# Kernel tuning notes

Hardware: AMD Instinct MI355X
Metric: run time of the kernel (lower is better)

The kernel has to match this reference:

```python
import jax, jax.numpy as jnp
import numpy as np

IN_DIM = 256
HID = 512
PAT = 10
B = 512
BN_EPS = 1e-5


def setup_inputs() -> dict:
    key = jax.random.key(0)
    ks = jax.random.split(key, 16)
    s = 0.05
    return {
        "x": jax.random.normal(ks[0], (B, IN_DIM), jnp.float32),
        # pattern_detector params
        "W1": jax.random.normal(ks[1], (HID, IN_DIM), jnp.float32) * s,
        "b1": jax.random.normal(ks[2], (HID,), jnp.float32) * s,
        "bn_gamma": 1.0 + jax.random.normal(ks[3], (HID,), jnp.float32) * s,
        "bn_beta": jax.random.normal(ks[4], (HID,), jnp.float32) * s,
        "bn_mean": jax.random.normal(ks[5], (HID,), jnp.float32) * s,
        "bn_var": jnp.ones((HID,), jnp.float32),
        "W2": jax.random.normal(ks[6], (HID // 2, HID), jnp.float32) * s,
        "b2": jax.random.normal(ks[7], (HID // 2,), jnp.float32) * s,
        "W3": jax.random.normal(ks[8], (PAT, HID // 2), jnp.float32) * s,
        "b3": jax.random.normal(ks[9], (PAT,), jnp.float32) * s,
        # similarity_layer params; first Linear weight [HID, 2*IN_DIM] split into
        # the half acting on x_i (Ws1_a) and the half acting on x_j (Ws1_b)
        "Ws1_a": jax.random.normal(ks[10], (HID, IN_DIM), jnp.float32) * s,
        "Ws1_b": jax.random.normal(ks[11], (HID, IN_DIM), jnp.float32) * s,
        "bs1": jax.random.normal(ks[12], (HID,), jnp.float32) * s,
        "ws2": jax.random.normal(ks[13], (HID,), jnp.float32) * s,
        "bs2": jax.random.normal(ks[14], (), jnp.float32) * s,
    }


def reference(x, W1, b1, bn_gamma, bn_beta, bn_mean, bn_var, W2, b2, W3, b3,
              Ws1_a, Ws1_b, bs1, ws2, bs2):
    # --- pattern_detector MLP (eval mode: BN uses running stats, dropout off) ---
    h = x @ W1.T + b1                                    # [B, HID]
    h = bn_gamma * (h - bn_mean) * jax.lax.rsqrt(bn_var + BN_EPS) + bn_beta
    h = jax.nn.relu(h)
    h2 = jax.nn.relu(h @ W2.T + b2)                      # [B, HID//2]
    pattern_scores = h2 @ W3.T + b3                      # [B, PAT]
    pattern_probs = jax.nn.softmax(pattern_scores, axis=-1)

    # --- pairwise similarity: sim(i,j) = MLP(concat(x_i, x_j)) ---
    # Linear([x_i; x_j]) = x_i @ Ws1_a^T + x_j @ Ws1_b^T + bs1, so precompute
    # the two GEMMs and broadcast-add instead of materializing [B,B,2*IN_DIM].
    A = x @ Ws1_a.T                                      # [B, HID]
    C = x @ Ws1_b.T                                      # [B, HID]
    hid = jax.nn.relu(A[:, None, :] + C[None, :, :] + bs1)  # [B, B, HID]
    logits = hid @ ws2 + bs2                             # [B, B]
    sim_full = jax.nn.sigmoid(logits)
    # Original loops i<j only and mirrors, diagonal stays 0. Results are
    # detached (.item()) in torch, so stop_gradient for faithfulness.
    iu = jnp.triu(jnp.ones((x.shape[0], x.shape[0]), sim_full.dtype), k=1)
    S = sim_full * iu
    similarities = jax.lax.stop_gradient(S + S.T)

    return pattern_probs, pattern_scores, similarities
```

## Files before the change

kernel.cpp:

```cpp
#include <hip/hip_runtime.h>
#include <math.h>

#define BN_EPS 1e-5f

typedef _Float16 half2v __attribute__((ext_vector_type(2)));
typedef _Float16 half8v __attribute__((ext_vector_type(8)));
typedef __fp16 fp16x8 __attribute__((ext_vector_type(8)));
typedef float floatx4 __attribute__((ext_vector_type(4)));

__device__ __forceinline__ float fdot2(half2v a, half2v b, float c) {
    return __builtin_amdgcn_fdot2(a, b, c, false);
}
__device__ __forceinline__ half2v cvt2(float a, float b) {
    return __builtin_bit_cast(half2v, __builtin_amdgcn_cvt_pkrtz(a, b));
}
__device__ __forceinline__ floatx4 mfma16(half8v a, half8v b, floatx4 c) {
    return __builtin_amdgcn_mfma_f32_16x16x32_f16(
        __builtin_bit_cast(fp16x8, a), __builtin_bit_cast(fp16x8, b), c, 0, 0, 0);
}
__device__ __forceinline__ half2v h2sub(half8v v, int s) {
    return __builtin_shufflevector(v, v, 0, 1);
}

__global__ __launch_bounds__(256) void fused3_mfma(
    const float* __restrict__ x,
    const float* __restrict__ W1, const float* __restrict__ b1,
    const float* __restrict__ g, const float* __restrict__ be,
    const float* __restrict__ mu, const float* __restrict__ va,
    const float* __restrict__ Wa, const float* __restrict__ bs1,
    const float* __restrict__ Wb,
    _Float16* __restrict__ h16, _Float16* __restrict__ A16,
    _Float16* __restrict__ C16)
{
    __shared__ _Float16 Xs[64][264];
    __shared__ _Float16 Ws[32][264];

    const int t  = threadIdx.x;
    const int n0 = blockIdx.x * 32;
    const int m0 = blockIdx.y * 64;
    const int z  = blockIdx.z;
    const float* __restrict__ Wp = (z == 0) ? W1 : (z == 1 ? Wa : Wb);

    #pragma unroll
    for (int i = 0; i < 16; ++i) {
        const int cidx = t + i * 256;
        const int row = cidx >> 6;
        const int c4  = cidx & 63;
        const float4 v = *(const float4*)&x[(m0 + row) * 256 + c4 * 4];
        *(half2v*)&Xs[row][c4 * 4 + 0] = cvt2(v.x, v.y);
        *(half2v*)&Xs[row][c4 * 4 + 2] = cvt2(v.z, v.w);
    }
    #pragma unroll
    for (int i = 0; i < 8; ++i) {
        const int cidx = t + i * 256;
        const int row = cidx >> 6;
        const int c4  = cidx & 63;
        const float4 v = *(const float4*)&Wp[(n0 + row) * 256 + c4 * 4];
        *(half2v*)&Ws[row][c4 * 4 + 0] = cvt2(v.x, v.y);
        *(half2v*)&Ws[row][c4 * 4 + 2] = cvt2(v.z, v.w);
    }
    __syncthreads();

    const int wave = t >> 6;
    const int lane = t & 63;
    const int wy = wave >> 1, wx = wave & 1;
    const int lrow = lane & 15;
    const int quad = lane >> 4;
    const int kq = quad * 8;

    floatx4 acc[2] = {{0.f, 0.f, 0.f, 0.f}, {0.f, 0.f, 0.f, 0.f}};

    #pragma unroll
    for (int kc = 0; kc < 256; kc += 32) {
        const half8v a0 = *(const half8v*)&Xs[wy * 32 + lrow][kc + kq];
        const half8v a1 = *(const half8v*)&Xs[wy * 32 + 16 + lrow][kc + kq];
        const half8v b0 = *(const half8v*)&Ws[wx * 16 + lrow][kc + kq];
        acc[0] = mfma16(a0, b0, acc[0]);
        acc[1] = mfma16(a1, b0, acc[1]);
    }

    const int n = n0 + wx * 16 + lrow;
    float scale, off;
    if (z == 0) {
        const float s = g[n] * rsqrtf(va[n] + BN_EPS);
        scale = s;
        off = (b1[n] - mu[n]) * s + be[n];
    } else if (z == 1) {
        scale = 1.f;
        off = bs1[n];
    } else {
        scale = 1.f;
        off = 0.f;
    }
    _Float16* __restrict__ dst = (z == 0) ? h16 : (z == 1 ? A16 : C16);
    #pragma unroll
    for (int mi = 0; mi < 2; ++mi) {
        #pragma unroll
        for (int r = 0; r < 4; ++r) {
            const int m = m0 + wy * 32 + mi * 16 + quad * 4 + r;
            float v = acc[mi][r] * scale + off;
            if (z == 0) v = fmaxf(v, 0.f);
            dst[m * 512 + n] = (_Float16)v;
        }
    }
}

__global__ __launch_bounds__(512) void h2sim_kernel(
    const _Float16* __restrict__ h16, const float* __restrict__ W2,
    const float* __restrict__ b2, float* __restrict__ h2o,
    const _Float16* __restrict__ A16, const _Float16* __restrict__ C16,
    const float* __restrict__ ws2, const float* __restrict__ bs2,
    float* __restrict__ S)
{
    __shared__ __align__(16) char smem[78080];
    const int bid = blockIdx.x;
    const int t   = threadIdx.x;

    if (bid < 128) {
        _Float16* Xs = (_Float16*)smem;
        _Float16* Ws = Xs + 32 * 520;
        float*    Ph = (float*)(smem + 66560);

        const int n0 = (bid & 7) * 32;
        const int m0 = (bid >> 3) * 32;

        #pragma unroll
        for (int i = 0; i < 4; ++i) {
            const int c = t + i * 512;
            const int row = c >> 6;
            const int c8  = c & 63;
            const float4 v = *(const float4*)&h16[(m0 + row) * 512 + c8 * 8];
            *(half8v*)&Xs[row * 520 + c8 * 8] = __builtin_bit_cast(half8v, v);
        }
        #pragma unroll
        for (int i = 0; i < 4; ++i) {
            const int c = t + i * 512;
            const int row = c >> 6;
            const int c8  = c & 63;
            const float4 v0 = *(const float4*)&W2[(n0 + row) * 512 + c8 * 8];
            const float4 v1 = *(const float4*)&W2[(n0 + row) * 512 + c8 * 8 + 4];
            _Float16* d = &Ws[row * 520 + c8 * 8];
            *(half2v*)(d + 0) = cvt2(v0.x, v0.y);
            *(half2v*)(d + 2) = cvt2(v0.z, v0.w);
            *(half2v*)(d + 4) = cvt2(v1.x, v1.y);
            *(half2v*)(d + 6) = cvt2(v1.z, v1.w);
        }
        __syncthreads();

        const int wave = t >> 6;
        const int lane = t & 63;
        const int gk = wave >> 2;
        const int wl = wave & 3;
        const int wy = wl >> 1, wx = wl & 1;
        const int lrow = lane & 15;
        const int quad = lane >> 4;
        const int kq = quad * 8;
        const int kb = gk * 256;

        floatx4 acc = {0.f, 0.f, 0.f, 0.f};
        #pragma unroll
        for (int kc = 0; kc < 256; kc += 32) {
            const half8v a = *(const half8v*)&Xs[(wy * 16 + lrow) * 520 + kb + kc + kq];
            const half8v b = *(const half8v*)&Ws[(wx * 16 + lrow) * 520 + kb + kc + kq];
            acc = mfma16(a, b, acc);
        }

        if (gk == 1) {
            #pragma unroll
            for (int r = 0; r < 4; ++r)
                Ph[(wy * 16 + quad * 4 + r) * 33 + wx * 16 + lrow] = acc[r];
        }
        __syncthreads();
        if (gk == 0) {
            const int n = n0 + wx * 16 + lrow;
            const float bb = b2[n];
            #pragma unroll
            for (int r = 0; r < 4; ++r) {
                const int ml = wy * 16 + quad * 4 + r;
                h2o[(m0 + ml) * 256 + n] =
                    fmaxf(acc[r] + Ph[ml * 33 + wx * 16 + lrow] + bb, 0.f);
            }
        }
        return;
    }

    _Float16* Rs = (_Float16*)smem;
    _Float16* Qs = Rs + 32 * 536;
    half2v*  wsh = (half2v*)(smem + 68608);
    float*   Psf = (float*)(smem + 68608 + 1024);
    float*   Tt  = Psf + 32 * 33;

    const int b = bid - 128;
    int jt = 0;
    while ((jt + 1) * (jt + 2) / 2 <= b) ++jt;
    const int it = b - jt * (jt + 1) / 2;
    const int r0 = it * 32, q0 = jt * 32;
    const bool diag = (it == jt);

    const int gk = t >> 8;
    const int tl = t & 255;
    const int tx = tl & 15, ty = tl >> 4;

    if (t < 256) {
        half2v w;
        w.x = (_Float16)ws2[2 * t];
        w.y = (_Float16)ws2[2 * t + 1];
        wsh[t] = w;
    }
    #pragma unroll
    for (int i = 0; i < 4; ++i) {
        const int c = t + i * 512;
        const int row = c >> 6;
        const int c8  = c & 63;
        const float4 vr = *(const float4*)&A16[(r0 + row) * 512 + c8 * 8];
        const float4 vq = *(const float4*)&C16[(q0 + row) * 512 + c8 * 8];
        *(half8v*)&Rs[row * 536 + c8 * 8] = __builtin_bit_cast(half8v, vr);
        *(half8v*)&Qs[row * 536 + c8 * 8] = __builtin_bit_cast(half8v, vq);
    }
    __syncthreads();

    const int cb = gk * 32;
    const half8v* rp0 = (const half8v*)&Rs[(ty * 2 + 0) * 536];
    const half8v* rp1 = (const half8v*)&Rs[(ty * 2 + 1) * 536];
    const half8v* qp0 = (const half8v*)&Qs[(tx * 2 + 0) * 536];
    const half8v* qp1 = (const half8v*)&Qs[(tx * 2 + 1) * 536];
    const half8v* wp8 = (const half8v*)wsh;
    const half2v z2 = {(_Float16)0, (_Float16)0};

    float a00 = 0.f, a01 = 0.f, a10 = 0.f, a11 = 0.f;
    #pragma unroll 4
    for (int c = 0; c < 32; ++c) {
        const half8v r0c = rp0[cb + c];
        const half8v r1c = rp1[cb + c];
        const half8v q0c = qp0[cb + c];
        const half8v q1c = qp1[cb + c];
        const half8v wc  = wp8[cb + c];
        #pragma unroll
        for (int s = 0; s < 4; ++s) {
            half2v r0s, r1s, q0s, q1s, wss;
            switch (s) {
            case 0: r0s = __builtin_shufflevector(r0c, r0c, 0, 1);
                    r1s = __builtin_shufflevector(r1c, r1c, 0, 1);
                    q0s = __builtin_shufflevector(q0c, q0c, 0, 1);
                    q1s = __builtin_shufflevector(q1c, q1c, 0, 1);
                    wss = __builtin_shufflevector(wc, wc, 0, 1); break;
            case 1: r0s = __builtin_shufflevector(r0c, r0c, 2, 3);
                    r1s = __builtin_shufflevector(r1c, r1c, 2, 3);
                    q0s = __builtin_shufflevector(q0c, q0c, 2, 3);
                    q1s = __builtin_shufflevector(q1c, q1c, 2, 3);
                    wss = __builtin_shufflevector(wc, wc, 2, 3); break;
            case 2: r0s = __builtin_shufflevector(r0c, r0c, 4, 5);
                    r1s = __builtin_shufflevector(r1c, r1c, 4, 5);
                    q0s = __builtin_shufflevector(q0c, q0c, 4, 5);
                    q1s = __builtin_shufflevector(q1c, q1c, 4, 5);
                    wss = __builtin_shufflevector(wc, wc, 4, 5); break;
            default: r0s = __builtin_shufflevector(r0c, r0c, 6, 7);
                    r1s = __builtin_shufflevector(r1c, r1c, 6, 7);
                    q0s = __builtin_shufflevector(q0c, q0c, 6, 7);
                    q1s = __builtin_shufflevector(q1c, q1c, 6, 7);
                    wss = __builtin_shufflevector(wc, wc, 6, 7); break;
            }
            a00 = fdot2(__builtin_elementwise_max(r0s + q0s, z2), wss, a00);
            a01 = fdot2(__builtin_elementwise_max(r0s + q1s, z2), wss, a01);
            a10 = fdot2(__builtin_elementwise_max(r1s + q0s, z2), wss, a10);
            a11 = fdot2(__builtin_elementwise_max(r1s + q1s, z2), wss, a11);
        }
    }

    if (gk == 1) {
        Psf[(ty * 2 + 0) * 33 + tx * 2 + 0] = a00;
        Psf[(ty * 2 + 0) * 33 + tx * 2 + 1] = a01;
        Psf[(ty * 2 + 1) * 33 + tx * 2 + 0] = a10;
        Psf[(ty * 2 + 1) * 33 + tx * 2 + 1] = a11;
    }
    __syncthreads();

    if (gk == 0) {
        const float bsv = bs2[0];
        float v[2][2];
        v[0][0] = a00 + Psf[(ty * 2 + 0) * 33 + tx * 2 + 0];
        v[0][1] = a01 + Psf[(ty * 2 + 0) * 33 + tx * 2 + 1];
        v[1][0] = a10 + Psf[(ty * 2 + 1) * 33 + tx * 2 + 0];
        v[1][1] = a11 + Psf[(ty * 2 + 1) * 33 + tx * 2 + 1];
        #pragma unroll
        for (int di = 0; di < 2; ++di)
            #pragma unroll
            for (int dj = 0; dj < 2; ++dj) {
                v[di][dj] = 1.f / (1.f + __expf(-(v[di][dj] + bsv)));
                Tt[(ty * 2 + di) * 33 + tx * 2 + dj] = v[di][dj];
            }
        if (!diag) {
            #pragma unroll
            for (int di = 0; di < 2; ++di)
                *(float2*)&S[(r0 + ty * 2 + di) * 512 + q0 + tx * 2] =
                    make_float2(v[di][0], v[di][1]);
        }
    }
    __syncthreads();

    if (gk == 0) {
        if (diag) {
            #pragma unroll
            for (int di = 0; di < 2; ++di)
                #pragma unroll
                for (int dj = 0; dj < 2; ++dj) {
                    const int rl = ty * 2 + di, ql = tx * 2 + dj;
                    const float o = rl < ql ? Tt[rl * 33 + ql]
                                  : (rl > ql ? Tt[ql * 33 + rl] : 0.f);
                    S[(r0 + rl) * 512 + q0 + ql] = o;
                }
        } else {
            #pragma unroll
            for (int di = 0; di < 2; ++di)
                #pragma unroll
                for (int dj = 0; dj < 2; ++dj)
                    S[(q0 + ty * 2 + di) * 512 + r0 + tx * 2 + dj] =
                        Tt[(tx * 2 + dj) * 33 + ty * 2 + di];
        }
    }
}

__global__ __launch_bounds__(256) void head_kernel(
    const float* __restrict__ h2, const float* __restrict__ W3,
    const float* __restrict__ b3, float* __restrict__ out)
{
    const int t = threadIdx.x;
    const int lane = t & 63;
    const int r = blockIdx.x * 4 + (t >> 6);

    float p[10];
    #pragma unroll
    for (int q = 0; q < 10; ++q) p[q] = 0.f;
    #pragma unroll
    for (int kk = 0; kk < 4; ++kk) {
        const int k = lane + kk * 64;
        const float hv = h2[r * 256 + k];
        #pragma unroll
        for (int q = 0; q < 10; ++q)
            p[q] = fmaf(hv, W3[q * 256 + k], p[q]);
    }
    #pragma unroll
    for (int q = 0; q < 10; ++q) {
        #pragma unroll
        for (int off = 32; off > 0; off >>= 1)
            p[q] += __shfl_down(p[q], off);
    }
    if (lane == 0) {
        float s[10], m = -1e30f;
        #pragma unroll
        for (int q = 0; q < 10; ++q) { s[q] = p[q] + b3[q]; m = fmaxf(m, s[q]); }
        float e[10], sum = 0.f;
        #pragma unroll
        for (int q = 0; q < 10; ++q) { e[q] = __expf(s[q] - m); sum += e[q]; }
        const float inv = 1.f / sum;
        #pragma unroll
        for (int q = 0; q < 10; ++q) {
            out[r * 10 + q] = e[q] * inv;
            out[5120 + r * 10 + q] = s[q];
        }
    }
}

extern "C" void kernel_launch(void* const* d_in, const int* in_sizes, int n_in,
                              void* d_out, int out_size, void* d_ws, size_t ws_size,
                              hipStream_t stream)
{
    const float* x   = (const float*)d_in[0];
    const float* W1  = (const float*)d_in[1];
    const float* b1  = (const float*)d_in[2];
    const float* g   = (const float*)d_in[3];
    const float* be  = (const float*)d_in[4];
    const float* mu  = (const float*)d_in[5];
    const float* va  = (const float*)d_in[6];
    const float* W2  = (const float*)d_in[7];
    const float* b2  = (const float*)d_in[8];
    const float* W3  = (const float*)d_in[9];
    const float* b3  = (const float*)d_in[10];
    const float* Wa  = (const float*)d_in[11];
    const float* Wb  = (const float*)d_in[12];
    const float* bs1 = (const float*)d_in[13];
    const float* ws2 = (const float*)d_in[14];
    const float* bs2 = (const float*)d_in[15];

    float* out = (float*)d_out;
    _Float16* h16 = (_Float16*)d_ws;
    float* h2 = (float*)(h16 + 512 * 512);
    _Float16* A16 = (_Float16*)(h2 + 512 * 256);
    _Float16* C16 = A16 + 512 * 512;

    fused3_mfma<<<dim3(16, 8, 3), 256, 0, stream>>>(x, W1, b1, g, be, mu, va,
                                                    Wa, bs1, Wb, h16, A16, C16);
    h2sim_kernel<<<264, 512, 0, stream>>>(h16, W2, b2, h2, A16, C16, ws2, bs2,
                                          out + 10240);
    head_kernel<<<128, 256, 0, stream>>>(h2, W3, b3, out);
}
```

Baseline: 101.7 us.

## Merge three kernels into one cooperative kernel with grid-wide syncs

Replaces the three separate launches (projection GEMMs, h2+similarity, head) with one cooperative mega-kernel of 256 blocks that uses grid.sync between phases. The first phase is retiled to 64x64 output tiles over 192 blocks. The second phase loops over its 264 jobs with 256 blocks, so 8 blocks run two jobs. The goal is to remove kernel launch gaps. In exchange it adds grid-barrier cost, a serialized tail in phase two, and a dependence on all 256 blocks of 512 threads with about 78KB of shared memory being co-resident.

After: 285.8 us. +181.0%, slower.

```diff
diff --git a/kernel.cpp b/kernel.cpp
--- a/kernel.cpp
+++ b/kernel.cpp
@@ -1,5 +1,8 @@
 #include <hip/hip_runtime.h>
+#include <hip/hip_cooperative_groups.h>
 #include <math.h>
+
+namespace cg = cooperative_groups;
 
 #define BN_EPS 1e-5f
 
@@ -18,345 +21,344 @@
     return __builtin_amdgcn_mfma_f32_16x16x32_f16(
         __builtin_bit_cast(fp16x8, a), __builtin_bit_cast(fp16x8, b), c, 0, 0, 0);
 }
-__device__ __forceinline__ half2v h2sub(half8v v, int s) {
-    return __builtin_shufflevector(v, v, 0, 1);
-}
-
-__global__ __launch_bounds__(256) void fused3_mfma(
+
+__global__ __launch_bounds__(512) void mega_kernel(
     const float* __restrict__ x,
     const float* __restrict__ W1, const float* __restrict__ b1,
     const float* __restrict__ g, const float* __restrict__ be,
     const float* __restrict__ mu, const float* __restrict__ va,
     const float* __restrict__ Wa, const float* __restrict__ bs1,
     const float* __restrict__ Wb,
+    const float* __restrict__ W2, const float* __restrict__ b2,
+    const float* __restrict__ W3, const float* __restrict__ b3,
+    const float* __restrict__ ws2, const float* __restrict__ bs2,
     _Float16* __restrict__ h16, _Float16* __restrict__ A16,
-    _Float16* __restrict__ C16)
-{
-    __shared__ _Float16 Xs[64][264];
-    __shared__ _Float16 Ws[32][264];
-
-    const int t  = threadIdx.x;
-    const int n0 = blockIdx.x * 32;
-    const int m0 = blockIdx.y * 64;
-    const int z  = blockIdx.z;
-    const float* __restrict__ Wp = (z == 0) ? W1 : (z == 1 ? Wa : Wb);
-
-    #pragma unroll
-    for (int i = 0; i < 16; ++i) {
-        const int cidx = t + i * 256;
-        const int row = cidx >> 6;
-        const int c4  = cidx & 63;
-        const float4 v = *(const float4*)&x[(m0 + row) * 256 + c4 * 4];
-        *(half2v*)&Xs[row][c4 * 4 + 0] = cvt2(v.x, v.y);
-        *(half2v*)&Xs[row][c4 * 4 + 2] = cvt2(v.z, v.w);
-    }
-    #pragma unroll
-    for (int i = 0; i < 8; ++i) {
-        const int cidx = t + i * 256;
-        const int row = cidx >> 6;
-        const int c4  = cidx & 63;
-        const float4 v = *(const float4*)&Wp[(n0 + row) * 256 + c4 * 4];
-        *(half2v*)&Ws[row][c4 * 4 + 0] = cvt2(v.x, v.y);
-        *(half2v*)&Ws[row][c4 * 4 + 2] = cvt2(v.z, v.w);
-    }
-    __syncthreads();
-
-    const int wave = t >> 6;
-    const int lane = t & 63;
-    const int wy = wave >> 1, wx = wave & 1;
-    const int lrow = lane & 15;
-    const int quad = lane >> 4;
-    const int kq = quad * 8;
-
-    floatx4 acc[2] = {{0.f, 0.f, 0.f, 0.f}, {0.f, 0.f, 0.f, 0.f}};
-
-    #pragma unroll
-    for (int kc = 0; kc < 256; kc += 32) {
-        const half8v a0 = *(const half8v*)&Xs[wy * 32 + lrow][kc + kq];
-        const half8v a1 = *(const half8v*)&Xs[wy * 32 + 16 + lrow][kc + kq];
-        const half8v b0 = *(const half8v*)&Ws[wx * 16 + lrow][kc + kq];
-        acc[0] = mfma16(a0, b0, acc[0]);
-        acc[1] = mfma16(a1, b0, acc[1]);
-    }
-
-    const int n = n0 + wx * 16 + lrow;
-    float scale, off;
-    if (z == 0) {
-        const float s = g[n] * rsqrtf(va[n] + BN_EPS);
-        scale = s;
-        off = (b1[n] - mu[n]) * s + be[n];
-    } else if (z == 1) {
-        scale = 1.f;
-        off = bs1[n];
-    } else {
-        scale = 1.f;
-        off = 0.f;
-    }
-    _Float16* __restrict__ dst = (z == 0) ? h16 : (z == 1 ? A16 : C16);
-    #pragma unroll
-    for (int mi = 0; mi < 2; ++mi) {
-        #pragma unroll
-        for (int r = 0; r < 4; ++r) {
-            const int m = m0 + wy * 32 + mi * 16 + quad * 4 + r;
-            float v = acc[mi][r] * scale + off;
-            if (z == 0) v = fmaxf(v, 0.f);
-            dst[m * 512 + n] = (_Float16)v;
-        }
-    }
-}
-
-__global__ __launch_bounds__(512) void h2sim_kernel(
-    const _Float16* __restrict__ h16, const float* __restrict__ W2,
-    const float* __restrict__ b2, float* __restrict__ h2o,
-    const _Float16* __restrict__ A16, const _Float16* __restrict__ C16,
-    const float* __restrict__ ws2, const float* __restrict__ bs2,
-    float* __restrict__ S)
+    _Float16* __restrict__ C16, float* __restrict__ h2o,
+    float* __restrict__ out)
 {
     __shared__ __align__(16) char smem[78080];
     const int bid = blockIdx.x;
     const int t   = threadIdx.x;
-
-    if (bid < 128) {
+    cg::grid_group grid = cg::this_grid();
+
+    if (bid < 192) {
         _Float16* Xs = (_Float16*)smem;
-        _Float16* Ws = Xs + 32 * 520;
-        float*    Ph = (float*)(smem + 66560);
-
-        const int n0 = (bid & 7) * 32;
-        const int m0 = (bid >> 3) * 32;
-
-        #pragma unroll
-        for (int i = 0; i < 4; ++i) {
+        _Float16* Ws = Xs + 64 * 264;
+        const int z   = bid / 64;
+        const int rem = bid % 64;
+        const int m0 = (rem >> 3) * 64;
+        const int n0 = (rem & 7) * 64;
+        const float* __restrict__ Wp = (z == 0) ? W1 : (z == 1 ? Wa : Wb);
+
+        #pragma unroll
+        for (int i = 0; i < 8; ++i) {
             const int c = t + i * 512;
             const int row = c >> 6;
-            const int c8  = c & 63;
-            const float4 v = *(const float4*)&h16[(m0 + row) * 512 + c8 * 8];
-            *(half8v*)&Xs[row * 520 + c8 * 8] = __builtin_bit_cast(half8v, v);
-        }
-        #pragma unroll
-        for (int i = 0; i < 4; ++i) {
+            const int c4  = c & 63;
+            const float4 v = *(const float4*)&x[(m0 + row) * 256 + c4 * 4];
+            *(half2v*)&Xs[row * 264 + c4 * 4 + 0] = cvt2(v.x, v.y);
+            *(half2v*)&Xs[row * 264 + c4 * 4 + 2] = cvt2(v.z, v.w);
+        }
+        #pragma unroll
+        for (int i = 0; i < 8; ++i) {
             const int c = t + i * 512;
             const int row = c >> 6;
-            const int c8  = c & 63;
-            const float4 v0 = *(const float4*)&W2[(n0 + row) * 512 + c8 * 8];
-            const float4 v1 = *(const float4*)&W2[(n0 + row) * 512 + c8 * 8 + 4];
-            _Float16* d = &Ws[row * 520 + c8 * 8];
-            *(half2v*)(d + 0) = cvt2(v0.x, v0.y);
-            *(half2v*)(d + 2) = cvt2(v0.z, v0.w);
-            *(half2v*)(d + 4) = cvt2(v1.x, v1.y);
-            *(half2v*)(d + 6) = cvt2(v1.z, v1.w);
+            const int c4  = c & 63;
+            const float4 v = *(const float4*)&Wp[(n0 + row) * 256 + c4 * 4];
+            *(half2v*)&Ws[row * 264 + c4 * 4 + 0] = cvt2(v.x, v.y);
+            *(half2v*)&Ws[row * 264 + c4 * 4 + 2] = cvt2(v.z, v.w);
         }
         __syncthreads();
 
         const int wave = t >> 6;
         const int lane = t & 63;
-        const int gk = wave >> 2;
-        const int wl = wave & 3;
-        const int wy = wl >> 1, wx = wl & 1;
+        const int wy = wave >> 2, wx = wave & 3;
         const int lrow = lane & 15;
         const int quad = lane >> 4;
         const int kq = quad * 8;
-        const int kb = gk * 256;
-
-        floatx4 acc = {0.f, 0.f, 0.f, 0.f};
+
+        floatx4 acc[2] = {{0.f, 0.f, 0.f, 0.f}, {0.f, 0.f, 0.f, 0.f}};
         #pragma unroll
         for (int kc = 0; kc < 256; kc += 32) {
-            const half8v a = *(const half8v*)&Xs[(wy * 16 + lrow) * 520 + kb + kc + kq];
-            const half8v b = *(const half8v*)&Ws[(wx * 16 + lrow) * 520 + kb + kc + kq];
-            acc = mfma16(a, b, acc);
-        }
-
-        if (gk == 1) {
-            #pragma unroll
-            for (int r = 0; r < 4; ++r)
-                Ph[(wy * 16 + quad * 4 + r) * 33 + wx * 16 + lrow] = acc[r];
-        }
+            const half8v a0 = *(const half8v*)&Xs[(wy * 32 + lrow) * 264 + kc + kq];
+            const half8v a1 = *(const half8v*)&Xs[(wy * 32 + 16 + lrow) * 264 + kc + kq];
+            const half8v b0 = *(const half8v*)&Ws[(wx * 16 + lrow) * 264 + kc + kq];
+            acc[0] = mfma16(a0, b0, acc[0]);
+            acc[1] = mfma16(a1, b0, acc[1]);
+        }
+
+        const int n = n0 + wx * 16 + lrow;
+        float scale, off;
+        if (z == 0) {
+            const float s = g[n] * rsqrtf(va[n] + BN_EPS);
+            scale = s;
+            off = (b1[n] - mu[n]) * s + be[n];
+        } else if (z == 1) {
+            scale = 1.f;
+            off = bs1[n];
+        } else {
+            scale = 1.f;
+            off = 0.f;
+        }
+        _Float16* __restrict__ dst = (z == 0) ? h16 : (z == 1 ? A16 : C16);
+        #pragma unroll
+        for (int mi = 0; mi < 2; ++mi) {
+            #pragma unroll
+            for (int r = 0; r < 4; ++r) {
+                const int m = m0 + wy * 32 + mi * 16 + quad * 4 + r;
+                float v = acc[mi][r] * scale + off;
+                if (z == 0) v = fmaxf(v, 0.f);
+                dst[m * 512 + n] = (_Float16)v;
+            }
+        }
+    }
+
+    __threadfence();
+    grid.sync();
+
+    float* __restrict__ S = out + 10240;
+    for (int job = bid; job < 264; job += 256) {
         __syncthreads();
-        if (gk == 0) {
-            const int n = n0 + wx * 16 + lrow;
-            const float bb = b2[n];
-            #pragma unroll
-            for (int r = 0; r < 4; ++r) {
-                const int ml = wy * 16 + quad * 4 + r;
-                h2o[(m0 + ml) * 256 + n] =
-                    fmaxf(acc[r] + Ph[ml * 33 + wx * 16 + lrow] + bb, 0.f);
-            }
-        }
-        return;
+        if (job < 128) {
+            _Float16* Xs = (_Float16*)smem;
+            _Float16* Ws = Xs + 32 * 520;
+            float*    Ph = (float*)(smem + 66560);
+
+            const int n0 = (job & 7) * 32;
+            const int m0 = (job >> 3) * 32;
+
+            #pragma unroll
+            for (int i = 0; i < 4; ++i) {
+                const int c = t + i * 512;
+                const int row = c >> 6;
+                const int c8  = c & 63;
+                const float4 v = *(const float4*)&h16[(m0 + row) * 512 + c8 * 8];
+                *(half8v*)&Xs[row * 520 + c8 * 8] = __builtin_bit_cast(half8v, v);
+            }
+            #pragma unroll
+            for (int i = 0; i < 4; ++i) {
+                const int c = t + i * 512;
+                const int row = c >> 6;
+                const int c8  = c & 63;
+                const float4 v0 = *(const float4*)&W2[(n0 + row) * 512 + c8 * 8];
+                const float4 v1 = *(const float4*)&W2[(n0 + row) * 512 + c8 * 8 + 4];
+                _Float16* d = &Ws[row * 520 + c8 * 8];
+                *(half2v*)(d + 0) = cvt2(v0.x, v0.y);
+                *(half2v*)(d + 2) = cvt2(v0.z, v0.w);
+                *(half2v*)(d + 4) = cvt2(v1.x, v1.y);
+                *(half2v*)(d + 6) = cvt2(v1.z, v1.w);
+            }
+            __syncthreads();
+
+            const int wave = t >> 6;
+            const int lane = t & 63;
+            const int gk = wave >> 2;
+            const int wl = wave & 3;
+            const int wy = wl >> 1, wx = wl & 1;
+            const int lrow = lane & 15;
+            const int quad = lane >> 4;
+            const int kq = quad * 8;
+            const int kb = gk * 256;
+
+            floatx4 acc = {0.f, 0.f, 0.f, 0.f};
+            #pragma unroll
+            for (int kc = 0; kc < 256; kc += 32) {
+                const half8v a = *(const half8v*)&Xs[(wy * 16 + lrow) * 520 + kb + kc + kq];
+                const half8v b = *(const half8v*)&Ws[(wx * 16 + lrow) * 520 + kb + kc + kq];
+                acc = mfma16(a, b, acc);
+            }
+
+            if (gk == 1) {
+                #pragma unroll
+                for (int r = 0; r < 4; ++r)
+                    Ph[(wy * 16 + quad * 4 + r) * 33 + wx * 16 + lrow] = acc[r];
+            }
+            __syncthreads();
+            if (gk == 0) {
+                const int n = n0 + wx * 16 + lrow;
+                const float bb = b2[n];
+                #pragma unroll
+                for (int r = 0; r < 4; ++r) {
+                    const int ml = wy * 16 + quad * 4 + r;
+                    h2o[(m0 + ml) * 256 + n] =
+                        fmaxf(acc[r] + Ph[ml * 33 + wx * 16 + lrow] + bb, 0.f);
+                }
+            }
+        } else {
+            _Float16* Rs = (_Float16*)smem;
+            _Float16* Qs = Rs + 32 * 536;
+            half2v*  wsh = (half2v*)(smem + 68608);
+            float*   Psf = (float*)(smem + 68608 + 1024);
+            float*   Tt  = Psf + 32 * 33;
+
+            const int b = job - 128;
+            int jt = 0;
+            while ((jt + 1) * (jt + 2) / 2 <= b) ++jt;
+            const int it = b - jt * (jt + 1) / 2;
+            const int r0 = it * 32, q0 = jt * 32;
+            const bool diag = (it == jt);
+
+            const int gk = t >> 8;
+            const int tl = t & 255;
+            const int tx = tl & 15, ty = tl >> 4;
+
+            if (t < 256) {
+                half2v w;
+                w.x = (_Float16)ws2[2 * t];
+                w.y = (_Float16)ws2[2 * t + 1];
+                wsh[t] = w;
+            }
+            #pragma unroll
+            for (int i = 0; i < 4; ++i) {
+                const int c = t + i * 512;
+                const int row = c >> 6;
+                const int c8  = c & 63;
+                const float4 vr = *(const float4*)&A16[(r0 + row) * 512 + c8 * 8];
+                const float4 vq = *(const float4*)&C16[(q0 + row) * 512 + c8 * 8];
+                *(half8v*)&Rs[row * 536 + c8 * 8] = __builtin_bit_cast(half8v, vr);
+                *(half8v*)&Qs[row * 536 + c8 * 8] = __builtin_bit_cast(half8v, vq);
+            }
+            __syncthreads();
+
+            const int cb = gk * 32;
+            const half8v* rp0 = (const half8v*)&Rs[(ty * 2 + 0) * 536];
+            const half8v* rp1 = (const half8v*)&Rs[(ty * 2 + 1) * 536];
+            const half8v* qp0 = (const half8v*)&Qs[(tx * 2 + 0) * 536];
+            const half8v* qp1 = (const half8v*)&Qs[(tx * 2 + 1) * 536];
+            const half8v* wp8 = (const half8v*)wsh;
+            const half2v z2 = {(_Float16)0, (_Float16)0};
+
+            float a00 = 0.f, a01 = 0.f, a10 = 0.f, a11 = 0.f;
+            #pragma unroll 4
+            for (int c = 0; c < 32; ++c) {
+                const half8v r0c = rp0[cb + c];
+                const half8v r1c = rp1[cb + c];
+                const half8v q0c = qp0[cb + c];
+                const half8v q1c = qp1[cb + c];
+                const half8v wc  = wp8[cb + c];
+                #pragma unroll
+                for (int s = 0; s < 4; ++s) {
+                    half2v r0s, r1s, q0s, q1s, wss;
+                    switch (s) {
+                    case 0: r0s = __builtin_shufflevector(r0c, r0c, 0, 1);
+                            r1s = __builtin_shufflevector(r1c, r1c, 0, 1);
+                            q0s = __builtin_shufflevector(q0c, q0c, 0, 1);
+                            q1s = __builtin_shufflevector(q1c, q1c, 0, 1);
+                            wss = __builtin_shufflevector(wc, wc, 0, 1); break;
+                    case 1: r0s = __builtin_shufflevector(r0c, r0c, 2, 3);
+                            r1s = __builtin_shufflevector(r1c, r1c, 2, 3);
+                            q0s = __builtin_shufflevector(q0c, q0c, 2, 3);
+                            q1s = __builtin_shufflevector(q1c, q1c, 2, 3);
+                            wss = __builtin_shufflevector(wc, wc, 2, 3); break;
+                    case 2: r0s = __builtin_shufflevector(r0c, r0c, 4, 5);
+                            r1s = __builtin_shufflevector(r1c, r1c, 4, 5);
+                            q0s = __builtin_shufflevector(q0c, q0c, 4, 5);
+                            q1s = __builtin_shufflevector(q1c, q1c, 4, 5);
+                            wss = __builtin_shufflevector(wc, wc, 4, 5); break;
+                    default: r0s = __builtin_shufflevector(r0c, r0c, 6, 7);
+                            r1s = __builtin_shufflevector(r1c, r1c, 6, 7);
+                            q0s = __builtin_shufflevector(q0c, q0c, 6, 7);
+                            q1s = __builtin_shufflevector(q1c, q1c, 6, 7);
+                            wss = __builtin_shufflevector(wc, wc, 6, 7); break;
+                    }
+                    a00 = fdot2(__builtin_elementwise_max(r0s + q0s, z2), wss, a00);
+                    a01 = fdot2(__builtin_elementwise_max(r0s + q1s, z2), wss, a01);
+                    a10 = fdot2(__builtin_elementwise_max(r1s + q0s, z2), wss, a10);
+                    a11 = fdot2(__builtin_elementwise_max(r1s + q1s, z2), wss, a11);
+                }
+            }
+
+            if (gk == 1) {
+                Psf[(ty * 2 + 0) * 33 + tx * 2 + 0] = a00;
+                Psf[(ty * 2 + 0) * 33 + tx * 2 + 1] = a01;
+                Psf[(ty * 2 + 1) * 33 + tx * 2 + 0] = a10;
+                Psf[(ty * 2 + 1) * 33 + tx * 2 + 1] = a11;
+            }
+            __syncthreads();
+
+            if (gk == 0) {
+                const float bsv = bs2[0];
+                float v[2][2];
+                v[0][0] = a00 + Psf[(ty * 2 + 0) * 33 + tx * 2 + 0];
+                v[0][1] = a01 + Psf[(ty * 2 + 0) * 33 + tx * 2 + 1];
+                v[1][0] = a10 + Psf[(ty * 2 + 1) * 33 + tx * 2 + 0];
+                v[1][1] = a11 + Psf[(ty * 2 + 1) * 33 + tx * 2 + 1];
+                #pragma unroll
+                for (int di = 0; di < 2; ++di)
+                    #pragma unroll
+                    for (int dj = 0; dj < 2; ++dj) {
+                        v[di][dj] = 1.f / (1.f + __expf(-(v[di][dj] + bsv)));
+                        Tt[(ty * 2 + di) * 33 + tx * 2 + dj] = v[di][dj];
+                    }
+                if (!diag) {
+                    #pragma unroll
+                    for (int di = 0; di < 2; ++di)
+                        *(float2*)&S[(r0 + ty * 2 + di) * 512 + q0 + tx * 2] =
+                            make_float2(v[di][0], v[di][1]);
+                }
+            }
+            __syncthreads();
+
+            if (gk == 0) {
+                if (diag) {
+                    #pragma unroll
+                    for (int di = 0; di < 2; ++di)
+                        #pragma unroll
+                        for (int dj = 0; dj < 2; ++dj) {
+                            const int rl = ty * 2 + di, ql = tx * 2 + dj;
+                            const float o = rl < ql ? Tt[rl * 33 + ql]
+                                          : (rl > ql ? Tt[ql * 33 + rl] : 0.f);
+                            S[(r0 + rl) * 512 + q0 + ql] = o;
+                        }
+                } else {
+                    #pragma unroll
+                    for (int di = 0; di < 2; ++di)
+                        #pragma unroll
+                        for (int dj = 0; dj < 2; ++dj)
+                            S[(q0 + ty * 2 + di) * 512 + r0 + tx * 2 + dj] =
+                                Tt[(tx * 2 + dj) * 33 + ty * 2 + di];
+                }
+            }
+        }
     }
 
-    _Float16* Rs = (_Float16*)smem;
-    _Float16* Qs = Rs + 32 * 536;
-    half2v*  wsh = (half2v*)(smem + 68608);
-    float*   Psf = (float*)(smem + 68608 + 1024);
-    float*   Tt  = Psf + 32 * 33;
-
-    const int b = bid - 128;
-    int jt = 0;
-    while ((jt + 1) * (jt + 2) / 2 <= b) ++jt;
-    const int it = b - jt * (jt + 1) / 2;
-    const int r0 = it * 32, q0 = jt * 32;
-    const bool diag = (it == jt);
-
-    const int gk = t >> 8;
-    const int tl = t & 255;
-    const int tx = tl & 15, ty = tl >> 4;
-
-    if (t < 256) {
-        half2v w;
-        w.x = (_Float16)ws2[2 * t];
-        w.y = (_Float16)ws2[2 * t + 1];
-        wsh[t] = w;
-    }
-    #pragma unroll
-    for (int i = 0; i < 4; ++i) {
-        const int c = t + i * 512;
-        const int row = c >> 6;
-        const int c8  = c & 63;
-        const float4 vr = *(const float4*)&A16[(r0 + row) * 512 + c8 * 8];
-        const float4 vq = *(const float4*)&C16[(q0 + row) * 512 + c8 * 8];
-        *(half8v*)&Rs[row * 536 + c8 * 8] = __builtin_bit_cast(half8v, vr);
-        *(half8v*)&Qs[row * 536 + c8 * 8] = __builtin_bit_cast(half8v, vq);
-    }
-    __syncthreads();
-
-    const int cb = gk * 32;
-    const half8v* rp0 = (const half8v*)&Rs[(ty * 2 + 0) * 536];
-    const half8v* rp1 = (const half8v*)&Rs[(ty * 2 + 1) * 536];
-    const half8v* qp0 = (const half8v*)&Qs[(tx * 2 + 0) * 536];
-    const half8v* qp1 = (const half8v*)&Qs[(tx * 2 + 1) * 536];
-    const half8v* wp8 = (const half8v*)wsh;
-    const half2v z2 = {(_Float16)0, (_Float16)0};
-
-    float a00 = 0.f, a01 = 0.f, a10 = 0.f, a11 = 0.f;
-    #pragma unroll 4
-    for (int c = 0; c < 32; ++c) {
-        const half8v r0c = rp0[cb + c];
-        const half8v r1c = rp1[cb + c];
-        const half8v q0c = qp0[cb + c];
-        const half8v q1c = qp1[cb + c];
-        const half8v wc  = wp8[cb + c];
-        #pragma unroll
-        for (int s = 0; s < 4; ++s) {
-            half2v r0s, r1s, q0s, q1s, wss;
-            switch (s) {
-            case 0: r0s = __builtin_shufflevector(r0c, r0c, 0, 1);
-                    r1s = __builtin_shufflevector(r1c, r1c, 0, 1);
-                    q0s = __builtin_shufflevector(q0c, q0c, 0, 1);
-                    q1s = __builtin_shufflevector(q1c, q1c, 0, 1);
-                    wss = __builtin_shufflevector(wc, wc, 0, 1); break;
-            case 1: r0s = __builtin_shufflevector(r0c, r0c, 2, 3);
-                    r1s = __builtin_shufflevector(r1c, r1c, 2, 3);
-                    q0s = __builtin_shufflevector(q0c, q0c, 2, 3);
-                    q1s = __builtin_shufflevector(q1c, q1c, 2, 3);
-                    wss = __builtin_shufflevector(wc, wc, 2, 3); break;
-            case 2: r0s = __builtin_shufflevector(r0c, r0c, 4, 5);
-                    r1s = __builtin_shufflevector(r1c, r1c, 4, 5);
-                    q0s = __builtin_shufflevector(q0c, q0c, 4, 5);
-                    q1s = __builtin_shufflevector(q1c, q1c, 4, 5);
-                    wss = __builtin_shufflevector(wc, wc, 4, 5); break;
-            default: r0s = __builtin_shufflevector(r0c, r0c, 6, 7);
-                    r1s = __builtin_shufflevector(r1c, r1c, 6, 7);
-                    q0s = __builtin_shufflevector(q0c, q0c, 6, 7);
-                    q1s = __builtin_shufflevector(q1c, q1c, 6, 7);
-                    wss = __builtin_shufflevector(wc, wc, 6, 7); break;
-            }
-            a00 = fdot2(__builtin_elementwise_max(r0s + q0s, z2), wss, a00);
-            a01 = fdot2(__builtin_elementwise_max(r0s + q1s, z2), wss, a01);
-            a10 = fdot2(__builtin_elementwise_max(r1s + q0s, z2), wss, a10);
-            a11 = fdot2(__builtin_elementwise_max(r1s + q1s, z2), wss, a11);
-        }
-    }
-
-    if (gk == 1) {
-        Psf[(ty * 2 + 0) * 33 + tx * 2 + 0] = a00;
-        Psf[(ty * 2 + 0) * 33 + tx * 2 + 1] = a01;
-        Psf[(ty * 2 + 1) * 33 + tx * 2 + 0] = a10;
-        Psf[(ty * 2 + 1) * 33 + tx * 2 + 1] = a11;
-    }
-    __syncthreads();
-
-    if (gk == 0) {
-        const float bsv = bs2[0];
-        float v[2][2];
-        v[0][0] = a00 + Psf[(ty * 2 + 0) * 33 + tx * 2 + 0];
-        v[0][1] = a01 + Psf[(ty * 2 + 0) * 33 + tx * 2 + 1];
-        v[1][0] = a10 + Psf[(ty * 2 + 1) * 33 + tx * 2 + 0];
-        v[1][1] = a11 + Psf[(ty * 2 + 1) * 33 + tx * 2 + 1];
-        #pragma unroll
-        for (int di = 0; di < 2; ++di)
-            #pragma unroll
-            for (int dj = 0; dj < 2; ++dj) {
-                v[di][dj] = 1.f / (1.f + __expf(-(v[di][dj] + bsv)));
-                Tt[(ty * 2 + di) * 33 + tx * 2 + dj] = v[di][dj];
-            }
-        if (!diag) {
-            #pragma unroll
-            for (int di = 0; di < 2; ++di)
-                *(float2*)&S[(r0 + ty * 2 + di) * 512 + q0 + tx * 2] =
-                    make_float2(v[di][0], v[di][1]);
-        }
-    }
-    __syncthreads();
-
-    if (gk == 0) {
-        if (diag) {
-            #pragma unroll
-            for (int di = 0; di < 2; ++di)
-                #pragma unroll
-                for (int dj = 0; dj < 2; ++dj) {
-                    const int rl = ty * 2 + di, ql = tx * 2 + dj;
-                    const float o = rl < ql ? Tt[rl * 33 + ql]
-                                  : (rl > ql ? Tt[ql * 33 + rl] : 0.f);
-                    S[(r0 + rl) * 512 + q0 + ql] = o;
-                }
-        } else {
-            #pragma unroll
-            for (int di = 0; di < 2; ++di)
-                #pragma unroll
-                for (int dj = 0; dj < 2; ++dj)
-                    S[(q0 + ty * 2 + di) * 512 + r0 + tx * 2 + dj] =
-                        Tt[(tx * 2 + dj) * 33 + ty * 2 + di];
-        }
-    }
-}
-
-__global__ __launch_bounds__(256) void head_kernel(
-    const float* __restrict__ h2, const float* __restrict__ W3,
-    const float* __restrict__ b3, float* __restrict__ out)
-{
-    const int t = threadIdx.x;
-    const int lane = t & 63;
-    const int r = blockIdx.x * 4 + (t >> 6);
-
-    float p[10];
-    #pragma unroll
-    for (int q = 0; q < 10; ++q) p[q] = 0.f;
-    #pragma unroll
-    for (int kk = 0; kk < 4; ++kk) {
-        const int k = lane + kk * 64;
-        const float hv = h2[r * 256 + k];
-        #pragma unroll
-        for (int q = 0; q < 10; ++q)
-            p[q] = fmaf(hv, W3[q * 256 + k], p[q]);
-    }
-    #pragma unroll
-    for (int q = 0; q < 10; ++q) {
-        #pragma unroll
-        for (int off = 32; off > 0; off >>= 1)
-            p[q] += __shfl_down(p[q], off);
-    }
-    if (lane == 0) {
-        float s[10], m = -1e30f;
-        #pragma unroll
-        for (int q = 0; q < 10; ++q) { s[q] = p[q] + b3[q]; m = fmaxf(m, s[q]); }
-        float e[10], sum = 0.f;
-        #pragma unroll
-        for (int q = 0; q < 10; ++q) { e[q] = __expf(s[q] - m); sum += e[q]; }
-        const float inv = 1.f / sum;
+    __threadfence();
+    grid.sync();
+
+    if (bid < 64) {
+        const int lane = t & 63;
+        const int r = bid * 8 + (t >> 6);
+
+        float p[10];
+        #pragma unroll
+        for (int q = 0; q < 10; ++q) p[q] = 0.f;
+        #pragma unroll
+        for (int kk = 0; kk < 4; ++kk) {
+            const int k = lane + kk * 64;
+            const float hv = h2o[r * 256 + k];
+            #pragma unroll
+            for (int q = 0; q < 10; ++q)
+                p[q] = fmaf(hv, W3[q * 256 + k], p[q]);
+        }
         #pragma unroll
         for (int q = 0; q < 10; ++q) {
-            out[r * 10 + q] = e[q] * inv;
-            out[5120 + r * 10 + q] = s[q];
+            #pragma unroll
+            for (int off = 32; off > 0; off >>= 1)
+                p[q] += __shfl_down(p[q], off);
+        }
+        if (lane == 0) {
+            float s[10], m = -1e30f;
+            #pragma unroll
+            for (int q = 0; q < 10; ++q) { s[q] = p[q] + b3[q]; m = fmaxf(m, s[q]); }
+            float e[10], sum = 0.f;
+            #pragma unroll
+            for (int q = 0; q < 10; ++q) { e[q] = __expf(s[q] - m); sum += e[q]; }
+            const float inv = 1.f / sum;
+            #pragma unroll
+            for (int q = 0; q < 10; ++q) {
+                out[r * 10 + q] = e[q] * inv;
+                out[5120 + r * 10 + q] = s[q];
+            }
         }
     }
 }
@@ -388,9 +390,13 @@
     _Float16* A16 = (_Float16*)(h2 + 512 * 256);
     _Float16* C16 = A16 + 512 * 512;
 
-    fused3_mfma<<<dim3(16, 8, 3), 256, 0, stream>>>(x, W1, b1, g, be, mu, va,
-                                                    Wa, bs1, Wb, h16, A16, C16);
-    h2sim_kernel<<<264, 512, 0, stream>>>(h16, W2, b2, h2, A16, C16, ws2, bs2,
-                                          out + 10240);
-    head_kernel<<<128, 256, 0, stream>>>(h2, W3, b3, out);
+    void* args[] = {
+        (void*)&x, (void*)&W1, (void*)&b1, (void*)&g, (void*)&be,
+        (void*)&mu, (void*)&va, (void*)&Wa, (void*)&bs1, (void*)&Wb,
+        (void*)&W2, (void*)&b2, (void*)&W3, (void*)&b3,
+        (void*)&ws2, (void*)&bs2,
+        (void*)&h16, (void*)&A16, (void*)&C16, (void*)&h2, (void*)&out
+    };
+    hipLaunchCooperativeKernel((const void*)mega_kernel, dim3(256), dim3(512),
+                               args, 0, stream);
 }
```
